# Kernel optimization log

Hardware: AMD Instinct MI355X
Metric: run time of the kernel (lower is better)

## Reference

```python
import jax, jax.numpy as jnp
import numpy as np

B, W, L, H = 50000, 100, 10, 10  # items, workers, labels, hidden_size
NEG = -99999999.0  # sentinel used by the original masking loop


def setup_inputs() -> dict:
    key = jax.random.key(0)
    k1, k2, k3, k4, k5 = jax.random.split(key, 5)
    hidden_sen = jax.random.normal(k1, (B, H), dtype=jnp.float32)
    # some workers did not label some items -> entire [b,w] row of crowd_mask is 0,
    # which makes crowd_s_worker (and hence att_weight) exactly 0 there
    labeled = jax.random.bernoulli(k2, 0.7, (B, W))[:, :, None].astype(jnp.float32)
    crowd_mask = jax.random.uniform(k3, (B, W, L), dtype=jnp.float32) * labeled
    worker_emb = jax.random.normal(k4, (W, H), dtype=jnp.float32)
    worker_abi = jax.random.normal(k5, (W, L, L), dtype=jnp.float32)
    return {"hidden_sen": hidden_sen, "crowd_mask": crowd_mask,
            "worker_emb": worker_emb, "worker_abi": worker_abi}


def reference(hidden_sen, crowd_mask, worker_emb, worker_abi):
    # att_weight = (hidden_sen @ W_emb^T) * sum_l crowd_mask   -> [B, W]
    crowd_s_worker = jnp.sum(crowd_mask, axis=2)
    att = jnp.matmul(hidden_sen, worker_emb.T) * crowd_s_worker
    # vectorized replacement of the nested Python loop: zeros -> large negative
    att = jnp.where(att == 0.0, NEG, att)
    att = jax.nn.softmax(att, axis=1)                      # [B, W]
    # f_score = att @ crowd_mask (per-item), squeezed       -> [B, L]
    f_score = jnp.einsum('bw,bwl->bl', att, crowd_mask)
    # Transform: softmax each worker's ability row, batched matmul over workers
    temp_abi = jax.nn.softmax(worker_abi, axis=2)          # [W, L, L]
    ob_labels = jnp.einsum('bl,wlm->bmw', f_score, temp_abi)  # [B, L, W]
    ob_labels_soft = jax.nn.softmax(ob_labels, axis=1)
    return (f_score, ob_labels, ob_labels_soft, att)
```

## Files before the change

kernel.cpp:

```cpp
#include <hip/hip_runtime.h>
#include <math.h>

constexpr int W_ = 100;
constexpr int L_ = 10;
constexpr int H_ = 10;
constexpr float NEGV = -99999999.0f;

__global__ __launch_bounds__(256, 4) void crowd_main_kernel(
    const float* __restrict__ hidden,
    const float* __restrict__ cmask,
    const float* __restrict__ wemb,
    const float* __restrict__ wabi,
    float* __restrict__ f_score,
    float* __restrict__ ob,
    float* __restrict__ obs,
    float* __restrict__ att_out,
    int B, int totalWaves)
{
    __shared__ float tabi[L_ * L_ * W_];

    for (int idx = threadIdx.x; idx < W_ * L_; idx += blockDim.x) {
        int w = idx / L_;
        int l = idx - w * L_;
        const float* row = wabi + (w * L_ + l) * L_;
        float v[L_];
        float mx = -INFINITY;
#pragma unroll
        for (int m = 0; m < L_; ++m) { v[m] = row[m]; mx = fmaxf(mx, v[m]); }
        float s = 0.f;
#pragma unroll
        for (int m = 0; m < L_; ++m) { v[m] = __expf(v[m] - mx); s += v[m]; }
        float inv = 1.0f / s;
#pragma unroll
        for (int m = 0; m < L_; ++m) tabi[(l * L_ + m) * W_ + w] = v[m] * inv;
    }
    __syncthreads();

    const int lane = threadIdx.x & 63;
    const int wave = blockIdx.x * (blockDim.x >> 6) + (threadIdx.x >> 6);
    const int w0 = lane;
    const int w1 = lane + 64;
    const bool has1 = (w1 < W_);
    const int w1m = has1 ? w1 : 0;

    float we0[H_], we1[H_];
#pragma unroll
    for (int h = 0; h < H_; ++h) we0[h] = wemb[w0 * H_ + h];
#pragma unroll
    for (int h = 0; h < H_; ++h) we1[h] = has1 ? wemb[w1 * H_ + h] : 0.f;

    for (int b = wave; b < B; b += totalWaves) {
        const float* hp = hidden + (size_t)b * H_;
        float hd[H_];
#pragma unroll
        for (int h = 0; h < H_; ++h) hd[h] = hp[h];

        const float* cb = cmask + (size_t)b * (W_ * L_);
        float cm0[L_], cm1[L_];
        {
            const float2* p0 = reinterpret_cast<const float2*>(cb + w0 * L_);
#pragma unroll
            for (int j = 0; j < L_ / 2; ++j) {
                float2 t = p0[j]; cm0[2 * j] = t.x; cm0[2 * j + 1] = t.y;
            }
        }
        if (has1) {
            const float2* p1 = reinterpret_cast<const float2*>(cb + w1 * L_);
#pragma unroll
            for (int j = 0; j < L_ / 2; ++j) {
                float2 t = p1[j]; cm1[2 * j] = t.x; cm1[2 * j + 1] = t.y;
            }
        } else {
#pragma unroll
            for (int j = 0; j < L_; ++j) cm1[j] = 0.f;
        }

        float cs0 = 0.f, cs1 = 0.f;
#pragma unroll
        for (int j = 0; j < L_; ++j) { cs0 += cm0[j]; cs1 += cm1[j]; }
        float d0 = 0.f, d1 = 0.f;
#pragma unroll
        for (int h = 0; h < H_; ++h) { d0 += hd[h] * we0[h]; d1 += hd[h] * we1[h]; }

        float a0 = d0 * cs0;
        float a1 = d1 * cs1;
        if (a0 == 0.f) a0 = NEGV;
        if (a1 == 0.f) a1 = NEGV;
        if (!has1) a1 = -INFINITY;

        float mx = fmaxf(a0, a1);
#pragma unroll
        for (int off = 32; off >= 1; off >>= 1) mx = fmaxf(mx, __shfl_xor(mx, off));

        float e0 = __expf(a0 - mx);
        float e1 = has1 ? __expf(a1 - mx) : 0.f;
        float s = e0 + e1;
#pragma unroll
        for (int off = 32; off >= 1; off >>= 1) s += __shfl_xor(s, off);
        float inv = 1.0f / s;
        float att0 = e0 * inv;
        float att1 = e1 * inv;

        att_out[(size_t)b * W_ + w0] = att0;
        if (has1) att_out[(size_t)b * W_ + w1] = att1;

        float fs[L_];
#pragma unroll
        for (int l = 0; l < L_; ++l) {
            float p = att0 * cm0[l] + att1 * cm1[l];
#pragma unroll
            for (int off = 32; off >= 1; off >>= 1) p += __shfl_xor(p, off);
            fs[l] = p;
        }
#pragma unroll
        for (int l = 0; l < L_; ++l)
            if (lane == l) f_score[(size_t)b * L_ + l] = fs[l];

        float ob0[L_], ob1[L_];
#pragma unroll
        for (int m = 0; m < L_; ++m) {
            float acc0 = 0.f, acc1 = 0.f;
#pragma unroll
            for (int l = 0; l < L_; ++l) {
                acc0 += fs[l] * tabi[(l * L_ + m) * W_ + w0];
                acc1 += fs[l] * tabi[(l * L_ + m) * W_ + w1m];
            }
            ob0[m] = acc0; ob1[m] = acc1;
        }

        float* obp  = ob  + (size_t)b * (L_ * W_);
        float* obsp = obs + (size_t)b * (L_ * W_);
#pragma unroll
        for (int m = 0; m < L_; ++m) {
            obp[m * W_ + w0] = ob0[m];
            if (has1) obp[m * W_ + w1] = ob1[m];
        }

        float mx0 = ob0[0], mx1 = ob1[0];
#pragma unroll
        for (int m = 1; m < L_; ++m) { mx0 = fmaxf(mx0, ob0[m]); mx1 = fmaxf(mx1, ob1[m]); }
        float s0 = 0.f, s1 = 0.f;
#pragma unroll
        for (int m = 0; m < L_; ++m) {
            ob0[m] = __expf(ob0[m] - mx0); s0 += ob0[m];
            ob1[m] = __expf(ob1[m] - mx1); s1 += ob1[m];
        }
        float i0 = 1.0f / s0, i1 = 1.0f / s1;
#pragma unroll
        for (int m = 0; m < L_; ++m) {
            obsp[m * W_ + w0] = ob0[m] * i0;
            if (has1) obsp[m * W_ + w1] = ob1[m] * i1;
        }
    }
}

extern "C" void kernel_launch(void* const* d_in, const int* in_sizes, int n_in,
                              void* d_out, int out_size, void* d_ws, size_t ws_size,
                              hipStream_t stream) {
    const float* hidden = (const float*)d_in[0];
    const float* cmask  = (const float*)d_in[1];
    const float* wemb   = (const float*)d_in[2];
    const float* wabi   = (const float*)d_in[3];

    const int B = in_sizes[0] / H_;

    float* f_score = (float*)d_out;
    float* ob      = f_score + (size_t)B * L_;
    float* obs     = ob + (size_t)B * L_ * W_;
    float* att     = obs + (size_t)B * L_ * W_;

    const int blocks = 2048;
    const int totalWaves = blocks * 4;
    crowd_main_kernel<<<blocks, 256, 0, stream>>>(
        hidden, cmask, wemb, wabi, f_score, ob, obs, att, B, totalWaves);
}
```

Measured before the change: 918.3 us.

## Stage per-wave outputs through LDS for coalesced float4 global stores

Each wave now writes its att, ob and ob_soft rows into a per-wave shared-memory staging buffer and then stores them to global memory as contiguous float4 chunks, replacing the scattered per-lane scalar stores. The hidden vector is also loaded as float2, and the launch changes to 512-thread blocks (8 waves) with 512 blocks. The goal is wider, fully coalesced stores on this store-heavy kernel. In exchange it adds LDS traffic, relies on compiler-only fences for intra-wave ordering, and halves the total wave count, which could lower occupancy.

```diff
diff --git a/kernel.cpp b/kernel.cpp
--- a/kernel.cpp
+++ b/kernel.cpp
@@ -6,7 +6,12 @@
 constexpr int H_ = 10;
 constexpr float NEGV = -99999999.0f;
 
-__global__ __launch_bounds__(256, 4) void crowd_main_kernel(
+constexpr int WAVES_PER_BLOCK = 8;
+constexpr int STAGE = 512;
+
+__device__ __forceinline__ void wave_fence() { asm volatile("" ::: "memory"); }
+
+__global__ __launch_bounds__(512, 4) void crowd_main_kernel(
     const float* __restrict__ hidden,
     const float* __restrict__ cmask,
     const float* __restrict__ wemb,
@@ -18,6 +23,7 @@
     int B, int totalWaves)
 {
     __shared__ float tabi[L_ * L_ * W_];
+    __shared__ float stagebuf[WAVES_PER_BLOCK][STAGE];
 
     for (int idx = threadIdx.x; idx < W_ * L_; idx += blockDim.x) {
         int w = idx / L_;
@@ -37,7 +43,10 @@
     __syncthreads();
 
     const int lane = threadIdx.x & 63;
-    const int wave = blockIdx.x * (blockDim.x >> 6) + (threadIdx.x >> 6);
+    const int wv = threadIdx.x >> 6;
+    const int wave = blockIdx.x * WAVES_PER_BLOCK + wv;
+    float* sb = stagebuf[wv];
+
     const int w0 = lane;
     const int w1 = lane + 64;
     const bool has1 = (w1 < W_);
@@ -50,10 +59,12 @@
     for (int h = 0; h < H_; ++h) we1[h] = has1 ? wemb[w1 * H_ + h] : 0.f;
 
     for (int b = wave; b < B; b += totalWaves) {
-        const float* hp = hidden + (size_t)b * H_;
+        const float2* hp2 = reinterpret_cast<const float2*>(hidden + (size_t)b * H_);
         float hd[H_];
 #pragma unroll
-        for (int h = 0; h < H_; ++h) hd[h] = hp[h];
+        for (int j = 0; j < H_ / 2; ++j) {
+            float2 t = hp2[j]; hd[2 * j] = t.x; hd[2 * j + 1] = t.y;
+        }
 
         const float* cb = cmask + (size_t)b * (W_ * L_);
         float cm0[L_], cm1[L_];
@@ -101,8 +112,14 @@
         float att0 = e0 * inv;
         float att1 = e1 * inv;
 
-        att_out[(size_t)b * W_ + w0] = att0;
-        if (has1) att_out[(size_t)b * W_ + w1] = att1;
+        sb[w0] = att0;
+        if (has1) sb[w1] = att1;
+        wave_fence();
+        if (lane < 25) {
+            float4 v = *reinterpret_cast<const float4*>(&sb[lane * 4]);
+            *reinterpret_cast<float4*>(att_out + (size_t)b * W_ + lane * 4) = v;
+        }
+        wave_fence();
 
         float fs[L_];
 #pragma unroll
@@ -130,10 +147,24 @@
 
         float* obp  = ob  + (size_t)b * (L_ * W_);
         float* obsp = obs + (size_t)b * (L_ * W_);
-#pragma unroll
-        for (int m = 0; m < L_; ++m) {
-            obp[m * W_ + w0] = ob0[m];
-            if (has1) obp[m * W_ + w1] = ob1[m];
+
+#pragma unroll
+        for (int h = 0; h < 2; ++h) {
+#pragma unroll
+            for (int mm = 0; mm < 5; ++mm) {
+                sb[mm * W_ + w0] = ob0[h * 5 + mm];
+                if (has1) sb[mm * W_ + w1] = ob1[h * 5 + mm];
+            }
+            wave_fence();
+            {
+                float4 v = *reinterpret_cast<const float4*>(&sb[lane * 4]);
+                *reinterpret_cast<float4*>(obp + h * 500 + lane * 4) = v;
+            }
+            if (lane < 61) {
+                float4 v = *reinterpret_cast<const float4*>(&sb[256 + lane * 4]);
+                *reinterpret_cast<float4*>(obp + h * 500 + 256 + lane * 4) = v;
+            }
+            wave_fence();
         }
 
         float mx0 = ob0[0], mx1 = ob1[0];
@@ -147,9 +178,25 @@
         }
         float i0 = 1.0f / s0, i1 = 1.0f / s1;
 #pragma unroll
-        for (int m = 0; m < L_; ++m) {
-            obsp[m * W_ + w0] = ob0[m] * i0;
-            if (has1) obsp[m * W_ + w1] = ob1[m] * i1;
+        for (int m = 0; m < L_; ++m) { ob0[m] *= i0; ob1[m] *= i1; }
+
+#pragma unroll
+        for (int h = 0; h < 2; ++h) {
+#pragma unroll
+            for (int mm = 0; mm < 5; ++mm) {
+                sb[mm * W_ + w0] = ob0[h * 5 + mm];
+                if (has1) sb[mm * W_ + w1] = ob1[h * 5 + mm];
+            }
+            wave_fence();
+            {
+                float4 v = *reinterpret_cast<const float4*>(&sb[lane * 4]);
+                *reinterpret_cast<float4*>(obsp + h * 500 + lane * 4) = v;
+            }
+            if (lane < 61) {
+                float4 v = *reinterpret_cast<const float4*>(&sb[256 + lane * 4]);
+                *reinterpret_cast<float4*>(obsp + h * 500 + 256 + lane * 4) = v;
+            }
+            wave_fence();
         }
     }
 }
@@ -169,8 +216,8 @@
     float* obs     = ob + (size_t)B * L_ * W_;
     float* att     = obs + (size_t)B * L_ * W_;
 
-    const int blocks = 2048;
-    const int totalWaves = blocks * 4;
-    crowd_main_kernel<<<blocks, 256, 0, stream>>>(
+    const int blocks = 512;
+    const int totalWaves = blocks * WAVES_PER_BLOCK;
+    crowd_main_kernel<<<blocks, 512, 0, stream>>>(
         hidden, cmask, wemb, wabi, f_score, ob, obs, att, B, totalWaves);
 }
```

Measured after the change: 1.020 ms. +11.1%, slower.
